# Performance work log

Measured on AMD Instinct MI355X. Metric: run time of the kernel, lower is better.

The kernel has to match this reference:

```python
import jax, jax.numpy as jnp
import numpy as np

B, L, E, MODES = 32, 2048, 512, 32  # batch, seq_len, d_model, kept Fourier modes (mode_select='low')


def setup_inputs() -> dict:
    key = jax.random.key(0)
    ks = jax.random.split(key, 6)
    scale = 1.0 / (E * E)  # FourierBlock scale = 1/(in_channels*out_channels), torch.rand init
    lin = E ** -0.5
    return {
        "queries": jax.random.normal(ks[0], (B, L, E), jnp.float32),
        "Wq": jax.random.normal(ks[1], (E, E), jnp.float32) * lin,
        "bq": jnp.zeros((E,), jnp.float32),
        "W1r": jax.random.uniform(ks[2], (E, E, MODES), jnp.float32) * scale,
        "W1i": jax.random.uniform(ks[3], (E, E, MODES), jnp.float32) * scale,
        "Wo": jax.random.normal(ks[4], (E, E), jnp.float32) * lin,
        "bo": jnp.zeros((E,), jnp.float32),
    }


def reference(queries, Wq, bq, W1r, W1i, Wo, bo):
    Bn, Ln, En = queries.shape
    # query projection
    q = queries @ Wq.T + bq                                    # (B, L, E)
    # FourierBlock: FFT along time, keep low `MODES` bins, complex channel mixing, inverse FFT
    xf = jnp.fft.rfft(q, axis=1)                               # (B, L//2+1, E) complex64
    W1 = (W1r + 1j * W1i).astype(jnp.complex64)                # (E_in, E_out, M)
    sel = xf[:, :MODES, :]                                     # (B, M, E) selected modes (mode_select='low')
    out_sel = jnp.einsum('bmi,iom->bmo', sel, W1)              # per-mode complex E x E mixing
    nfreq = Ln // 2 + 1
    out_ft = jnp.zeros((Bn, nfreq, En), jnp.complex64).at[:, :MODES, :].set(out_sel)
    x = jnp.fft.irfft(out_ft, n=Ln, axis=1)                    # (B, L, E) real
    # output projection (attn is None in the original; return the tensor output)
    return x @ Wo.T + bo
```

## Files before the change

### kernel.cpp

```cpp
#include <hip/hip_runtime.h>
#include <hip/hip_bf16.h>

typedef _Float16 f16;
typedef _Float16 f16x8 __attribute__((ext_vector_type(8)));
typedef _Float16 f16x4 __attribute__((ext_vector_type(4)));
typedef float f32x4 __attribute__((ext_vector_type(4)));

#define QPAD 136
#define PADK2 72

#define W1SCALE 262144.0f
#define W1DESCALE 3.814697265625e-06f

static __device__ __forceinline__ f32x4 mfma16(f16x8 a, f16x8 b, f32x4 c) {
  return __builtin_amdgcn_mfma_f32_16x16x32_f16(a, b, c, 0, 0, 0);
}

__global__ __launch_bounds__(256) void k_prep(f16* __restrict__ FhT, f16* __restrict__ Gh,
                                              const float* __restrict__ Wq,
                                              const float* __restrict__ Wo,
                                              f16* __restrict__ Wq16,
                                              f16* __restrict__ Wo16) {
  int idx = blockIdx.x * 256 + threadIdx.x;
  const float w = 6.28318530717958647692f / 2048.0f;
  {
    int k2 = idx >> 11, l = idx & 2047;
    int k = k2 & 31;
    float th = (float)((k * l) & 2047) * w;
    float v = (k2 < 32) ? cosf(th) : -sinf(th);
    FhT[k2 * 2048 + l] = (f16)v;
  }
  {
    int l = idx >> 6, kk = idx & 63;
    int k = kk & 31;
    float th = (float)((k * l) & 2047) * w;
    float v;
    if (kk < 32) v = ((k == 0) ? 1.0f : 2.0f) * (1.0f / 2048.0f) * cosf(th);
    else         v = (k == 0) ? 0.0f : (-2.0f / 2048.0f) * sinf(th);
    Gh[l * 64 + kk] = (f16)v;
  }
  {
    const float* src = (idx < 65536) ? Wq : Wo;
    f16* dst = (idx < 65536) ? Wq16 : Wo16;
    int i = idx & 65535;
    float4 v = ((const float4*)src)[i];
    f16x4 o = {(f16)v.x, (f16)v.y, (f16)v.z, (f16)v.w};
    *(f16x4*)(dst + (size_t)i * 4) = o;
  }
}

__global__ __launch_bounds__(256) void k_dft_fwd(const f16* __restrict__ FhT,
                                                 const float* __restrict__ queries,
                                                 f16* __restrict__ p16) {
  __shared__ __align__(16) f16 As[64 * QPAD];
  __shared__ __align__(16) f16 Bs[64 * QPAD];
  const int n0 = blockIdx.x * 64;
  const int b  = blockIdx.y;
  const int kb = blockIdx.z * 512;
  const int t = threadIdx.x;
  const int wid = t >> 6, lane = t & 63;
  const int mh = wid & 1, nh = wid >> 1;
  const int l15 = lane & 15, kq = lane >> 4;
  const int arow = t >> 2, ac0 = (t & 3) << 5;
  const int bcol = t & 63, bkg = t >> 6;

  float qv[32];
  f16x8 av[4];

  auto issue = [&](int ph) {
    const int k0 = kb + ph * 128;
    const float* qp = queries + ((size_t)b * 2048 + k0 + bkg * 32) * 512 + n0 + bcol;
#pragma unroll
    for (int r = 0; r < 32; ++r) qv[r] = qp[(size_t)r * 512];
#pragma unroll
    for (int j = 0; j < 4; ++j)
      av[j] = *(const f16x8*)(FhT + (size_t)arow * 2048 + k0 + ac0 + j * 8);
  };

  issue(0);
  f32x4 acc[2][2] = {};
  for (int ph = 0; ph < 4; ++ph) {
    __syncthreads();
#pragma unroll
    for (int j = 0; j < 4; ++j)
      *(f16x8*)(As + arow * QPAD + ac0 + j * 8) = av[j];
#pragma unroll
    for (int s = 0; s < 4; ++s) {
      f16x8 pk = {(f16)qv[s*8+0], (f16)qv[s*8+1], (f16)qv[s*8+2], (f16)qv[s*8+3],
                  (f16)qv[s*8+4], (f16)qv[s*8+5], (f16)qv[s*8+6], (f16)qv[s*8+7]};
      *(f16x8*)(Bs + bcol * QPAD + bkg * 32 + s * 8) = pk;
    }
    __syncthreads();
    if (ph < 3) issue(ph + 1);
#pragma unroll
    for (int ks = 0; ks < 4; ++ks) {
      const int kofs = ks * 32 + kq * 8;
      f16x8 a0 = *(const f16x8*)(As + (mh * 32 + 0  + l15) * QPAD + kofs);
      f16x8 a1 = *(const f16x8*)(As + (mh * 32 + 16 + l15) * QPAD + kofs);
      f16x8 b0 = *(const f16x8*)(Bs + (nh * 32 + 0  + l15) * QPAD + kofs);
      f16x8 b1 = *(const f16x8*)(Bs + (nh * 32 + 16 + l15) * QPAD + kofs);
      acc[0][0] = mfma16(a0, b0, acc[0][0]);
      acc[0][1] = mfma16(a0, b1, acc[0][1]);
      acc[1][0] = mfma16(a1, b0, acc[1][0]);
      acc[1][1] = mfma16(a1, b1, acc[1][1]);
    }
  }
#pragma unroll
  for (int mf = 0; mf < 2; ++mf)
#pragma unroll
    for (int nf = 0; nf < 2; ++nf)
#pragma unroll
      for (int r = 0; r < 4; ++r) {
        int k2 = mh * 32 + mf * 16 + kq * 4 + r;
        int col = n0 + nh * 32 + nf * 16 + l15;
        p16[((size_t)blockIdx.z * 2048 + b * 64 + k2) * 512 + col] = (f16)acc[mf][nf][r];
      }
}

template <int NP>
__global__ __launch_bounds__(256) void k_reduceN16(const f16* __restrict__ p,
                                                   f16* __restrict__ dst) {
  size_t i8 = ((size_t)blockIdx.x * 256 + threadIdx.x) * 8;
  f16x8 v[NP];
#pragma unroll
  for (int c = 0; c < NP; ++c)
    v[c] = *(const f16x8*)(p + (size_t)c * 1048576 + i8);
  f16x8 s = v[0];
#pragma unroll
  for (int c = 1; c < NP; ++c) s = s + v[c];
  *(f16x8*)(dst + i8) = s;
}

__global__ __launch_bounds__(256) void k_gemm_nk(const f16* __restrict__ A,
                                                 const f16* __restrict__ Bnk,
                                                 f16* __restrict__ C,
                                                 const float* __restrict__ bias0,
                                                 float bscale, int selt) {
  __shared__ __align__(16) f16 As[64 * QPAD];
  __shared__ __align__(16) f16 Bs[32 * QPAD];
  const int n0 = blockIdx.x * 32, m0 = blockIdx.y * 64;
  const int t = threadIdx.x;
  const int wid = t >> 6, lane = t & 63;
  const int mh = wid & 1, nh = wid >> 1;
  const int l15 = lane & 15, kq = lane >> 4;
  const int row = t >> 2, c0 = (t & 3) << 5;
  f32x4 acc[2] = {};
  for (int ph = 0; ph < 4; ++ph) {
    const int k0 = ph * 128;
    __syncthreads();
#pragma unroll
    for (int j = 0; j < 4; ++j)
      *(f16x8*)(As + row * QPAD + c0 + j * 8) =
          *(const f16x8*)(A + (size_t)(m0 + row) * 512 + k0 + c0 + j * 8);
    if (t < 128) {
      const int br = t >> 2, bc0 = (t & 3) << 5;
#pragma unroll
      for (int j = 0; j < 4; ++j)
        *(f16x8*)(Bs + br * QPAD + bc0 + j * 8) =
            *(const f16x8*)(Bnk + (size_t)(n0 + br) * 512 + k0 + bc0 + j * 8);
    }
    __syncthreads();
#pragma unroll
    for (int ks = 0; ks < 4; ++ks) {
      const int kofs = ks * 32 + kq * 8;
      f16x8 a0 = *(const f16x8*)(As + (mh * 32 + 0  + l15) * QPAD + kofs);
      f16x8 a1 = *(const f16x8*)(As + (mh * 32 + 16 + l15) * QPAD + kofs);
      f16x8 b0 = *(const f16x8*)(Bs + (nh * 16 + l15) * QPAD + kofs);
      acc[0] = mfma16(a0, b0, acc[0]);
      acc[1] = mfma16(a1, b0, acc[1]);
    }
  }
#pragma unroll
  for (int mf = 0; mf < 2; ++mf)
#pragma unroll
    for (int r = 0; r < 4; ++r) {
      int mg = m0 + mh * 32 + mf * 16 + kq * 4 + r;
      int col = n0 + nh * 16 + l15;
      float cv = acc[mf][r];
      if (bias0 != nullptr && (mg & 63) == 0) cv += bscale * bias0[col];
      size_t didx = selt ? (((size_t)(mg & 63) * 32 + (mg >> 6)) * 512 + col)
                         : ((size_t)mg * 512 + col);
      C[didx] = (f16)cv;
    }
}

__global__ __launch_bounds__(512) void k_modes_fused(const float* __restrict__ W1r,
                                                     const float* __restrict__ W1i,
                                                     const f16* __restrict__ selT,
                                                     f16* __restrict__ pmode) {
  __shared__ __align__(16) f16 Wst[2][16][648];
  const int o0 = blockIdx.x * 16, m0 = blockIdx.y * 16, is = blockIdx.z;
  const int t = threadIdx.x;
  const int lane = t & 63, wv = t >> 6;
  const int l15 = lane & 15, kq = lane >> 4, kofs = kq << 3;
  const int mq = t & 3, p = t >> 2;
  const int soo = p & 15, sib = p >> 4;
  f32x4 accR[2][2] = {}, accI[2][2] = {};
  const int ibase = is * 64;
  for (int ch = 0; ch < 2; ++ch) {
    const int i0c = ibase + ch * 32;
    __syncthreads();
#pragma unroll
    for (int ri = 0; ri < 2; ++ri) {
      const float* src = ri ? W1i : W1r;
#pragma unroll
      for (int qq = 0; qq < 4; ++qq) {
        int ii = sib + 8 * qq;
        const float4 v = *(const float4*)(src + (size_t)(i0c + ii) * 16384 +
                                          (o0 + soo) * 32 + m0 + mq * 4);
        f16* wp = &Wst[ri][mq * 4][soo * 40 + ii];
        wp[0 * 648] = (f16)(W1SCALE * v.x);
        wp[1 * 648] = (f16)(W1SCALE * v.y);
        wp[2 * 648] = (f16)(W1SCALE * v.z);
        wp[3 * 648] = (f16)(W1SCALE * v.w);
      }
    }
    __syncthreads();
#pragma unroll
    for (int ml = 0; ml < 2; ++ml) {
      const int mloc = 2 * wv + ml;
      const int mg = m0 + mloc;
      f16x8 ar0 = *(const f16x8*)(selT + ((size_t)mg * 32 + 0  + l15) * 512 + i0c + kofs);
      f16x8 ar1 = *(const f16x8*)(selT + ((size_t)mg * 32 + 16 + l15) * 512 + i0c + kofs);
      f16x8 ai0 = *(const f16x8*)(selT + ((size_t)(32 + mg) * 32 + 0  + l15) * 512 + i0c + kofs);
      f16x8 ai1 = *(const f16x8*)(selT + ((size_t)(32 + mg) * 32 + 16 + l15) * 512 + i0c + kofs);
      f16x8 br = *(const f16x8*)(&Wst[0][mloc][l15 * 40 + kofs]);
      f16x8 bi = *(const f16x8*)(&Wst[1][mloc][l15 * 40 + kofs]);
      f16x8 ain0 = -ai0, ain1 = -ai1;
      accR[ml][0] = mfma16(ar0,  br, accR[ml][0]);
      accR[ml][0] = mfma16(ain0, bi, accR[ml][0]);
      accI[ml][0] = mfma16(ar0,  bi, accI[ml][0]);
      accI[ml][0] = mfma16(ai0,  br, accI[ml][0]);
      accR[ml][1] = mfma16(ar1,  br, accR[ml][1]);
      accR[ml][1] = mfma16(ain1, bi, accR[ml][1]);
      accI[ml][1] = mfma16(ar1,  bi, accI[ml][1]);
      accI[ml][1] = mfma16(ai1,  br, accI[ml][1]);
    }
  }
#pragma unroll
  for (int ml = 0; ml < 2; ++ml) {
    const int mg = m0 + 2 * wv + ml;
#pragma unroll
    for (int bt = 0; bt < 2; ++bt)
#pragma unroll
      for (int r = 0; r < 4; ++r) {
        int bb = bt * 16 + kq * 4 + r;
        int og = o0 + l15;
        pmode[((size_t)is * 2048 + bb * 64 + mg) * 512 + og]      = (f16)accR[ml][bt][r];
        pmode[((size_t)is * 2048 + bb * 64 + 32 + mg) * 512 + og] = (f16)accI[ml][bt][r];
      }
  }
}

__global__ __launch_bounds__(256) void k_dft_inv(const f16* __restrict__ Gh,
                                                 const f16* __restrict__ u,
                                                 const float* __restrict__ bo,
                                                 float* __restrict__ out) {
  __shared__ __align__(16) f16 As[64 * PADK2];
  __shared__ __align__(16) f16 Bs[64 * PADK2];
  const int n0 = blockIdx.x * 64, l0 = blockIdx.y * 64, b = blockIdx.z;
  const int t = threadIdx.x, wid = t >> 6, lane = t & 63;
  const int mh = wid & 1, nh = wid >> 1;
#pragma unroll
  for (int p = 0; p < 2; ++p) {
    int v = t + 256 * p, row = v >> 3, c8 = (v & 7) << 3;
    *(f16x8*)(As + row * PADK2 + c8) = *(const f16x8*)(Gh + (size_t)(l0 + row) * 64 + c8);
  }
  {
    int col = t & 63, kg = t >> 6;
    const f16* up = u + ((size_t)b * 64 + kg * 16) * 512 + n0 + col;
    f16 vv[16];
#pragma unroll
    for (int s = 0; s < 16; ++s) vv[s] = up[(size_t)s * 512];
#pragma unroll
    for (int s4 = 0; s4 < 4; ++s4) {
      f16x4 pk = {vv[s4 * 4], vv[s4 * 4 + 1], vv[s4 * 4 + 2], vv[s4 * 4 + 3]};
      *(f16x4*)(Bs + col * PADK2 + kg * 16 + s4 * 4) = pk;
    }
  }
  __syncthreads();
  f32x4 acc[2][2] = {};
#pragma unroll
  for (int ks = 0; ks < 2; ++ks) {
    const int kofs = ks * 32 + ((lane >> 4) << 3);
    f16x8 a0 = *(const f16x8*)(As + (mh * 32 + 0  + (lane & 15)) * PADK2 + kofs);
    f16x8 a1 = *(const f16x8*)(As + (mh * 32 + 16 + (lane & 15)) * PADK2 + kofs);
    f16x8 b0 = *(const f16x8*)(Bs + (nh * 32 + 0  + (lane & 15)) * PADK2 + kofs);
    f16x8 b1 = *(const f16x8*)(Bs + (nh * 32 + 16 + (lane & 15)) * PADK2 + kofs);
    acc[0][0] = mfma16(a0, b0, acc[0][0]);
    acc[0][1] = mfma16(a0, b1, acc[0][1]);
    acc[1][0] = mfma16(a1, b0, acc[1][0]);
    acc[1][1] = mfma16(a1, b1, acc[1][1]);
  }
#pragma unroll
  for (int mf = 0; mf < 2; ++mf)
#pragma unroll
    for (int nf = 0; nf < 2; ++nf)
#pragma unroll
      for (int r = 0; r < 4; ++r) {
        int l = l0 + mh * 32 + mf * 16 + ((lane >> 4) << 2) + r;
        int col = n0 + nh * 32 + nf * 16 + (lane & 15);
        float cv = acc[mf][nf][r] * W1DESCALE + bo[col];
        out[((size_t)b * 2048 + l) * 512 + col] = cv;
      }
}

extern "C" void kernel_launch(void* const* d_in, const int* in_sizes, int n_in,
                              void* d_out, int out_size, void* d_ws, size_t ws_size,
                              hipStream_t stream) {
  const float* queries = (const float*)d_in[0];
  const float* Wq      = (const float*)d_in[1];
  const float* bq      = (const float*)d_in[2];
  const float* W1r     = (const float*)d_in[3];
  const float* W1i     = (const float*)d_in[4];
  const float* Wo      = (const float*)d_in[5];
  const float* bo      = (const float*)d_in[6];
  float* out           = (float*)d_out;

  char* ws = (char*)d_ws;
  size_t off = 0;
  auto alloc = [&](size_t bytes) {
    off = (off + 255) & ~(size_t)255;
    char* p = ws + off;
    off += bytes;
    return p;
  };
  f16* FhT    = (f16*)alloc((size_t)64 * 2048 * 2);
  f16* Gh     = (f16*)alloc((size_t)2048 * 64 * 2);
  f16* Wq16   = (f16*)alloc((size_t)512 * 512 * 2);
  f16* Wo16   = (f16*)alloc((size_t)512 * 512 * 2);
  f16* p16    = (f16*)alloc((size_t)4 * 2048 * 512 * 2);
  f16* t16    = (f16*)alloc((size_t)2048 * 512 * 2);
  f16* selT   = (f16*)alloc((size_t)2048 * 512 * 2);
  f16* pmode  = (f16*)alloc((size_t)8 * 2048 * 512 * 2);
  f16* osel   = (f16*)alloc((size_t)2048 * 512 * 2);
  f16* u16    = (f16*)alloc((size_t)2048 * 512 * 2);

  hipLaunchKernelGGL(k_prep, dim3(512), dim3(256), 0, stream, FhT, Gh, Wq, Wo, Wq16, Wo16);
  hipLaunchKernelGGL(k_dft_fwd, dim3(8, 32, 4), dim3(256), 0, stream, FhT, queries, p16);
  hipLaunchKernelGGL(k_reduceN16<4>, dim3(512), dim3(256), 0, stream, p16, t16);
  hipLaunchKernelGGL(k_gemm_nk, dim3(16, 32), dim3(256), 0, stream, t16, Wq16, selT,
                     bq, 2048.0f, 1);
  hipLaunchKernelGGL(k_modes_fused, dim3(32, 2, 8), dim3(512), 0, stream,
                     W1r, W1i, selT, pmode);
  hipLaunchKernelGGL(k_reduceN16<8>, dim3(512), dim3(256), 0, stream, pmode, osel);
  hipLaunchKernelGGL(k_gemm_nk, dim3(16, 32), dim3(256), 0, stream, osel, Wo16, u16,
                     (const float*)nullptr, 0.0f, 0);
  hipLaunchKernelGGL(k_dft_inv, dim3(8, 32, 32), dim3(256), 0, stream, Gh, u16, bo, out);
}
```

Measured before the change: 125.6 us.

## Fuse split-K partial reductions into GEMM A-tile loads and halve modes split

Removes both standalone reduce kernels by summing the split-K partial buffers while loading the A tile inside the GEMM, which now uses 512 threads with one MFMA tile per wave. The modes kernel's input-channel split drops from 8 to 4 slices (4 chunks each), halving partial buffer traffic. This saves two launches and the round trip through intermediate buffers, but each GEMM block re-reads the partials for every N tile, and the modes kernel has half as many blocks.

```diff
diff --git a/kernel.cpp b/kernel.cpp
--- a/kernel.cpp
+++ b/kernel.cpp
@@ -118,70 +118,59 @@
 }
 
 template <int NP>
-__global__ __launch_bounds__(256) void k_reduceN16(const f16* __restrict__ p,
-                                                   f16* __restrict__ dst) {
-  size_t i8 = ((size_t)blockIdx.x * 256 + threadIdx.x) * 8;
-  f16x8 v[NP];
-#pragma unroll
-  for (int c = 0; c < NP; ++c)
-    v[c] = *(const f16x8*)(p + (size_t)c * 1048576 + i8);
-  f16x8 s = v[0];
-#pragma unroll
-  for (int c = 1; c < NP; ++c) s = s + v[c];
-  *(f16x8*)(dst + i8) = s;
-}
-
-__global__ __launch_bounds__(256) void k_gemm_nk(const f16* __restrict__ A,
-                                                 const f16* __restrict__ Bnk,
-                                                 f16* __restrict__ C,
-                                                 const float* __restrict__ bias0,
-                                                 float bscale, int selt) {
+__global__ __launch_bounds__(512) void k_gemm_red(const f16* __restrict__ P,
+                                                  const f16* __restrict__ Bnk,
+                                                  f16* __restrict__ C,
+                                                  const float* __restrict__ bias0,
+                                                  float bscale, int selt) {
   __shared__ __align__(16) f16 As[64 * QPAD];
   __shared__ __align__(16) f16 Bs[32 * QPAD];
   const int n0 = blockIdx.x * 32, m0 = blockIdx.y * 64;
   const int t = threadIdx.x;
-  const int wid = t >> 6, lane = t & 63;
-  const int mh = wid & 1, nh = wid >> 1;
+  const int wv = t >> 6, lane = t & 63;
+  const int mh = wv & 3, nh = wv >> 2;
   const int l15 = lane & 15, kq = lane >> 4;
-  const int row = t >> 2, c0 = (t & 3) << 5;
-  f32x4 acc[2] = {};
+  const int arow = t >> 3, ac0 = (t & 7) << 4;
+  const int brow = t >> 4, bc0 = (t & 15) << 3;
+  f32x4 acc = {};
   for (int ph = 0; ph < 4; ++ph) {
     const int k0 = ph * 128;
     __syncthreads();
-#pragma unroll
-    for (int j = 0; j < 4; ++j)
-      *(f16x8*)(As + row * QPAD + c0 + j * 8) =
-          *(const f16x8*)(A + (size_t)(m0 + row) * 512 + k0 + c0 + j * 8);
-    if (t < 128) {
-      const int br = t >> 2, bc0 = (t & 3) << 5;
-#pragma unroll
-      for (int j = 0; j < 4; ++j)
-        *(f16x8*)(Bs + br * QPAD + bc0 + j * 8) =
-            *(const f16x8*)(Bnk + (size_t)(n0 + br) * 512 + k0 + bc0 + j * 8);
-    }
+    f16x8 v[2][NP];
+    const size_t aidx = (size_t)(m0 + arow) * 512 + k0 + ac0;
+#pragma unroll
+    for (int h = 0; h < 2; ++h)
+#pragma unroll
+      for (int c = 0; c < NP; ++c)
+        v[h][c] = *(const f16x8*)(P + (size_t)c * 1048576 + aidx + h * 8);
+    f16x8 bv = *(const f16x8*)(Bnk + (size_t)(n0 + brow) * 512 + k0 + bc0);
+#pragma unroll
+    for (int h = 0; h < 2; ++h) {
+      f16x8 s = v[h][0];
+#pragma unroll
+      for (int c = 1; c < NP; ++c) s = s + v[h][c];
+      *(f16x8*)(As + arow * QPAD + ac0 + h * 8) = s;
+    }
+    *(f16x8*)(Bs + brow * QPAD + bc0) = bv;
     __syncthreads();
 #pragma unroll
     for (int ks = 0; ks < 4; ++ks) {
       const int kofs = ks * 32 + kq * 8;
-      f16x8 a0 = *(const f16x8*)(As + (mh * 32 + 0  + l15) * QPAD + kofs);
-      f16x8 a1 = *(const f16x8*)(As + (mh * 32 + 16 + l15) * QPAD + kofs);
-      f16x8 b0 = *(const f16x8*)(Bs + (nh * 16 + l15) * QPAD + kofs);
-      acc[0] = mfma16(a0, b0, acc[0]);
-      acc[1] = mfma16(a1, b0, acc[1]);
-    }
-  }
-#pragma unroll
-  for (int mf = 0; mf < 2; ++mf)
-#pragma unroll
-    for (int r = 0; r < 4; ++r) {
-      int mg = m0 + mh * 32 + mf * 16 + kq * 4 + r;
-      int col = n0 + nh * 16 + l15;
-      float cv = acc[mf][r];
-      if (bias0 != nullptr && (mg & 63) == 0) cv += bscale * bias0[col];
-      size_t didx = selt ? (((size_t)(mg & 63) * 32 + (mg >> 6)) * 512 + col)
-                         : ((size_t)mg * 512 + col);
-      C[didx] = (f16)cv;
-    }
+      f16x8 a = *(const f16x8*)(As + (mh * 16 + l15) * QPAD + kofs);
+      f16x8 b = *(const f16x8*)(Bs + (nh * 16 + l15) * QPAD + kofs);
+      acc = mfma16(a, b, acc);
+    }
+  }
+#pragma unroll
+  for (int r = 0; r < 4; ++r) {
+    int mg = m0 + mh * 16 + kq * 4 + r;
+    int col = n0 + nh * 16 + l15;
+    float cv = acc[r];
+    if (bias0 != nullptr && (mg & 63) == 0) cv += bscale * bias0[col];
+    size_t didx = selt ? (((size_t)(mg & 63) * 32 + (mg >> 6)) * 512 + col)
+                       : ((size_t)mg * 512 + col);
+    C[didx] = (f16)cv;
+  }
 }
 
 __global__ __launch_bounds__(512) void k_modes_fused(const float* __restrict__ W1r,
@@ -196,8 +185,8 @@
   const int mq = t & 3, p = t >> 2;
   const int soo = p & 15, sib = p >> 4;
   f32x4 accR[2][2] = {}, accI[2][2] = {};
-  const int ibase = is * 64;
-  for (int ch = 0; ch < 2; ++ch) {
+  const int ibase = is * 128;
+  for (int ch = 0; ch < 4; ++ch) {
     const int i0c = ibase + ch * 32;
     __syncthreads();
 #pragma unroll
@@ -330,21 +319,17 @@
   f16* Wq16   = (f16*)alloc((size_t)512 * 512 * 2);
   f16* Wo16   = (f16*)alloc((size_t)512 * 512 * 2);
   f16* p16    = (f16*)alloc((size_t)4 * 2048 * 512 * 2);
-  f16* t16    = (f16*)alloc((size_t)2048 * 512 * 2);
   f16* selT   = (f16*)alloc((size_t)2048 * 512 * 2);
-  f16* pmode  = (f16*)alloc((size_t)8 * 2048 * 512 * 2);
-  f16* osel   = (f16*)alloc((size_t)2048 * 512 * 2);
+  f16* pmode  = (f16*)alloc((size_t)4 * 2048 * 512 * 2);
   f16* u16    = (f16*)alloc((size_t)2048 * 512 * 2);
 
   hipLaunchKernelGGL(k_prep, dim3(512), dim3(256), 0, stream, FhT, Gh, Wq, Wo, Wq16, Wo16);
   hipLaunchKernelGGL(k_dft_fwd, dim3(8, 32, 4), dim3(256), 0, stream, FhT, queries, p16);
-  hipLaunchKernelGGL(k_reduceN16<4>, dim3(512), dim3(256), 0, stream, p16, t16);
-  hipLaunchKernelGGL(k_gemm_nk, dim3(16, 32), dim3(256), 0, stream, t16, Wq16, selT,
+  hipLaunchKernelGGL(k_gemm_red<4>, dim3(16, 32), dim3(512), 0, stream, p16, Wq16, selT,
                      bq, 2048.0f, 1);
-  hipLaunchKernelGGL(k_modes_fused, dim3(32, 2, 8), dim3(512), 0, stream,
+  hipLaunchKernelGGL(k_modes_fused, dim3(32, 2, 4), dim3(512), 0, stream,
                      W1r, W1i, selT, pmode);
-  hipLaunchKernelGGL(k_reduceN16<8>, dim3(512), dim3(256), 0, stream, pmode, osel);
-  hipLaunchKernelGGL(k_gemm_nk, dim3(16, 32), dim3(256), 0, stream, osel, Wo16, u16,
+  hipLaunchKernelGGL(k_gemm_red<4>, dim3(16, 32), dim3(512), 0, stream, pmode, Wo16, u16,
                      (const float*)nullptr, 0.0f, 0);
   hipLaunchKernelGGL(k_dft_inv, dim3(8, 32, 32), dim3(256), 0, stream, Gh, u16, bo, out);
 }
```

Result: no change. 124.0 us, median of 2 (-1.3%).
